# Kernel tuning notes

Hardware: AMD Instinct MI355X
Metric: run time of the kernel (lower is better)

## Reference

```python
import jax, jax.numpy as jnp
import numpy as np

B, T, V, D, H, HS, FF, L = 4, 1024, 32000, 1024, 16, 64, 4096, 8
STD = 0.02

def _ln(x, g, b, eps=1e-5):
    m = x.mean(-1, keepdims=True)
    v = ((x - m) ** 2).mean(-1, keepdims=True)
    return (x - m) / jnp.sqrt(v + eps) * g + b

def setup_inputs() -> dict:
    key = jax.random.key(0)
    ks = jax.random.split(key, 16)
    n = lambda k, shp: jax.random.normal(k, shp, dtype=jnp.float32) * STD
    inp = {
        "idx": jax.random.randint(ks[0], (B, T), 0, V),
        "tok_emb": n(ks[1], (V, D)),
        "pos_emb": n(ks[2], (T, D)),
        # per-layer stacked attention weights; [D, H, HS] per layer (no bias)
        "Wq": n(ks[3], (L, D, H, HS)),
        "Wk": n(ks[4], (L, D, H, HS)),
        "Wv": n(ks[5], (L, D, H, HS)),
        "Wp": n(ks[6], (L, H * HS, D)),
        "bp": jnp.zeros((L, D), jnp.float32),
        "ln1_g": jnp.ones((L, D), jnp.float32),
        "ln1_b": jnp.zeros((L, D), jnp.float32),
        "ln2_g": jnp.ones((L, D), jnp.float32),
        "ln2_b": jnp.zeros((L, D), jnp.float32),
        "W1": n(ks[7], (L, D, FF)),
        "b1": jnp.zeros((L, FF), jnp.float32),
        "W2": n(ks[8], (L, FF, D)),
        "b2": jnp.zeros((L, D), jnp.float32),
        "lnf_g": jnp.ones((D,), jnp.float32),
        "lnf_b": jnp.zeros((D,), jnp.float32),
        "Wlm": n(ks[9], (D, V)),
        "blm": jnp.zeros((V,), jnp.float32),
    }
    return inp

def reference(idx, tok_emb, pos_emb, Wq, Wk, Wv, Wp, bp, ln1_g, ln1_b,
              ln2_g, ln2_b, W1, b1, W2, b2, lnf_g, lnf_b, Wlm, blm):
    Bb, Tt = idx.shape
    x = tok_emb[idx] + pos_emb[:Tt]                      # [B,T,D]
    causal = jnp.tril(jnp.ones((Tt, Tt), bool))          # tril mask
    for l in range(L):
        xn = _ln(x, ln1_g[l], ln1_b[l])
        q = jnp.einsum('btd,dhk->bhtk', xn, Wq[l])
        k = jnp.einsum('btd,dhk->bhtk', xn, Wk[l])
        v = jnp.einsum('btd,dhk->bhtk', xn, Wv[l])
        w = jnp.einsum('bhtk,bhsk->bhts', q, k) * (HS ** -0.5)
        w = jnp.where(causal, w, -jnp.inf)
        w = jax.nn.softmax(w, axis=-1)
        o = jnp.einsum('bhts,bhsk->bhtk', w, v)
        o = o.transpose(0, 2, 1, 3).reshape(Bb, Tt, H * HS)  # concat heads
        x = x + o @ Wp[l] + bp[l]
        xn = _ln(x, ln2_g[l], ln2_b[l])
        x = x + jax.nn.relu(xn @ W1[l] + b1[l]) @ W2[l] + b2[l]
    x = _ln(x, lnf_g, lnf_b)
    logits = x @ Wlm + blm                               # [B,T,V]
    return logits
```

## Files before the change

kernel.cpp:

```cpp
#include <hip/hip_runtime.h>
#include <cstdint>

typedef __attribute__((ext_vector_type(4))) float f32x4;
typedef __attribute__((ext_vector_type(8))) short s16x8;
typedef __attribute__((ext_vector_type(4))) short s16x4;
typedef unsigned short u16;
typedef unsigned int u32;
typedef __attribute__((address_space(1))) void gas_void;
typedef __attribute__((address_space(3))) void las_void;

#define B_ 4
#define T_ 1024
#define V_ 32000
#define D_ 1024
#define H_ 16
#define HS_ 64
#define FF_ 4096
#define L_ 8
#define BT_ (B_ * T_)

__device__ __forceinline__ float bf2f(u16 h) { return __uint_as_float(((u32)h) << 16); }
__device__ __forceinline__ u16 f2bf(float f) {
  u32 u = __float_as_uint(f);
  u += 0x7fffu + ((u >> 16) & 1u);
  return (u16)(u >> 16);
}

__device__ __forceinline__ void gld16(const void* g, void* l) {
  __builtin_amdgcn_global_load_lds((gas_void*)(uintptr_t)g,
                                   (las_void*)(u32)(uintptr_t)l, 16, 0, 0);
}


template <int EPI>
__global__ __launch_bounds__(512, 2) void gemm256(
    const u16* __restrict__ A, const u16* __restrict__ Bt,
    const float* __restrict__ bias, float* Cf, u16* Cb,
    int M, int N, int K, int nrowb) {
  __shared__ u16 lds[2][2][2][8192];
  const int tid = threadIdx.x;
  const int lane = tid & 63;
  const int lr = lane & 15, hi = lane >> 4;
  const int wid = tid >> 6;
  const int wm128 = (wid >> 2) << 7;
  const int wn64 = (wid & 3) << 6;
  const int logical = ((int)blockIdx.x & 7) * ((int)gridDim.x >> 3) + ((int)blockIdx.x >> 3);
  const int row0 = (logical % nrowb) << 8;
  const int col0 = (logical / nrowb) << 8;
  const int NT = K >> 6;
  const int srow = tid >> 2;
  const int schunk = tid & 3;
  const int xo = ((hi + (lr >> 1)) & 3) << 4;

  f32x4 acc[32];
#pragma unroll
  for (int i = 0; i < 32; ++i) acc[i] = f32x4{0.f, 0.f, 0.f, 0.f};
  s16x8 bfr[4];

#define VMW(N) asm volatile("s_waitcnt vmcnt(" #N ")" ::: "memory")

#define STG(DB, DK, OP, KT)                                                    \
  {                                                                            \
    const u16* sp_ = (OP) ? Bt : A;                                            \
    const int base_ = (OP) ? col0 : row0;                                      \
    const int c0_ = ((KT) << 6) + ((DK) << 5);                                 \
    _Pragma("unroll")                                                          \
    for (int sh_ = 0; sh_ < 2; ++sh_) {                                        \
      const int rr_ = (sh_ << 7) + srow;                                       \
      const int ko_ = ((schunk - (rr_ >> 1)) & 3) << 3;                        \
      gld16(sp_ + (size_t)(base_ + rr_) * K + c0_ + ko_,                       \
            (char*)&lds[DB][DK][OP][0] + (sh_ << 13) + (wid << 10));           \
    }                                                                          \
  }

#define PHASE(BUF, MH, KS, LOADB, STG_STMT, VM_STMT)                           \
  {                                                                            \
    __builtin_amdgcn_sched_barrier(0);                                         \
    const char* As_ = (const char*)&lds[BUF][KS][0][0];                        \
    const char* Bs_ = (const char*)&lds[BUF][KS][1][0];                        \
    const int ra_ = wm128 + ((MH) << 6) + lr;                                  \
    s16x8 af_[4];                                                              \
    _Pragma("unroll")                                                          \
    for (int q_ = 0; q_ < 4; ++q_)                                             \
      af_[q_] = *(const s16x8*)(As_ + ((ra_ + (q_ << 4)) << 6) + xo);          \
    if (LOADB) {                                                               \
      _Pragma("unroll")                                                        \
      for (int q_ = 0; q_ < 4; ++q_)                                           \
        bfr[q_] = *(const s16x8*)(Bs_ + ((wn64 + lr + (q_ << 4)) << 6) + xo);  \
    }                                                                          \
    STG_STMT;                                                                  \
    __builtin_amdgcn_sched_barrier(0);                                         \
    __builtin_amdgcn_s_barrier();                                              \
    asm volatile("s_waitcnt lgkmcnt(0)" ::: "memory");                         \
    __builtin_amdgcn_sched_barrier(0);                                         \
    __builtin_amdgcn_s_setprio(1);                                             \
    _Pragma("unroll")                                                          \
    for (int mi_ = 0; mi_ < 4; ++mi_) {                                        \
      _Pragma("unroll")                                                        \
      for (int nj_ = 0; nj_ < 4; ++nj_)                                        \
        acc[((MH)*4 + mi_) * 4 + nj_] = __builtin_amdgcn_mfma_f32_16x16x32_bf16( \
            af_[mi_], bfr[nj_], acc[((MH)*4 + mi_) * 4 + nj_], 0, 0, 0);       \
    }                                                                          \
    __builtin_amdgcn_s_setprio(0);                                             \
    __builtin_amdgcn_sched_barrier(0);                                         \
    VM_STMT;                                                                   \
    __builtin_amdgcn_s_barrier();                                              \
  }

  STG(0, 0, 0, 0)
  STG(0, 0, 1, 0)
  STG(0, 1, 0, 0)
  STG(0, 1, 1, 0)
  STG(1, 0, 0, 1)
  STG(1, 0, 1, 1)
  VMW(8);
  __builtin_amdgcn_s_barrier();

  const int NI = NT >> 1;
  for (int it = 0; it < NI - 1; ++it) {
    const int t1 = 2 * it + 1, t2 = 2 * it + 2, t3 = 2 * it + 3;
    PHASE(0, 0, 0, 1, STG(1, 1, 0, t1), )
    PHASE(0, 1, 0, 0, STG(1, 1, 1, t1), VMW(6))
    PHASE(0, 0, 1, 1, STG(0, 0, 0, t2), )
    PHASE(0, 1, 1, 0, STG(0, 0, 1, t2), VMW(6))
    PHASE(1, 0, 0, 1, STG(0, 1, 0, t2), )
    PHASE(1, 1, 0, 0, STG(0, 1, 1, t2), VMW(6))
    PHASE(1, 0, 1, 1, STG(1, 0, 0, t3), )
    PHASE(1, 1, 1, 0, STG(1, 0, 1, t3), VMW(6))
  }
  {
    PHASE(0, 0, 0, 1, STG(1, 1, 0, NT - 1), )
    PHASE(0, 1, 0, 0, STG(1, 1, 1, NT - 1), VMW(8))
    PHASE(0, 0, 1, 1, (void)0, )
    PHASE(0, 1, 1, 0, (void)0, VMW(4))
    PHASE(1, 0, 0, 1, (void)0, )
    PHASE(1, 1, 0, 0, (void)0, VMW(0))
    PHASE(1, 0, 1, 1, (void)0, )
    PHASE(1, 1, 1, 0, (void)0, )
  }
#undef PHASE
#undef STG
#undef VMW

  const int gr0 = row0 + wm128;
  const int gc0 = col0 + wn64;
#pragma unroll
  for (int nj = 0; nj < 4; ++nj) {
    const int col = gc0 + (nj << 4) + lr;
    const float bv = (EPI != 0) ? bias[col] : 0.f;
#pragma unroll
    for (int mi = 0; mi < 8; ++mi) {
#pragma unroll
      for (int rg = 0; rg < 4; ++rg) {
        const int row = gr0 + (mi << 4) + (hi << 2) + rg;
        const size_t off = (size_t)row * N + col;
        float val = acc[mi * 4 + nj][rg] + bv;
        if constexpr (EPI == 2) val = fmaxf(val, 0.f);
        if constexpr (EPI == 0 || EPI == 2) Cb[off] = f2bf(val);
        else Cf[off] = val;
      }
    }
  }
}

template <int EPI>
__global__ __launch_bounds__(256) void gemm_bt(
    const u16* __restrict__ A, const u16* __restrict__ Bt,
    const float* __restrict__ bias, float* Cf, u16* Cb,
    int M, int N, int K) {
  __shared__ u16 lds[2][2][4096];
  const int tid = threadIdx.x;
  const int lane = tid & 63;
  const int lr = lane & 15, hi = lane >> 4;
  const int wid = tid >> 6;
  const int wm = wid >> 1, wn = wid & 1;
  const int row0 = blockIdx.y << 7, col0 = blockIdx.x << 7;
  const int NT = K >> 5;
  const int wbase = (tid & ~63) << 4;
  const int xo = ((hi + (lr >> 1)) & 3) << 4;

  f32x4 acc[4][4];
#pragma unroll
  for (int i = 0; i < 4; ++i)
#pragma unroll
    for (int j = 0; j < 4; ++j) acc[i][j] = f32x4{0.f, 0.f, 0.f, 0.f};

  auto stage = [&](int buf, int kt) {
#pragma unroll
    for (int c = 0; c < 2; ++c) {
      const int o = (c << 12) + (tid << 4);
      const int r = o >> 6;
      const int ko = ((((o >> 4) & 3) - (r >> 1)) & 3) << 3;
      gld16(A + (size_t)(row0 + r) * K + (kt << 5) + ko,
            (char*)&lds[buf][0][0] + (c << 12) + wbase);
      gld16(Bt + (size_t)(col0 + r) * K + (kt << 5) + ko,
            (char*)&lds[buf][1][0] + (c << 12) + wbase);
    }
  };

  stage(0, 0);
  __syncthreads();
  int cur = 0;
  for (int kt = 0; kt < NT; ++kt) {
    if (kt + 1 < NT) stage(cur ^ 1, kt + 1);
    const char* As = (const char*)&lds[cur][0][0];
    const char* Bs = (const char*)&lds[cur][1][0];
    s16x8 af[4], bfr[4];
#pragma unroll
    for (int i = 0; i < 4; ++i) {
      const int ra = (wm << 6) + (i << 4) + lr;
      af[i] = *(const s16x8*)(As + (ra << 6) + xo);
      const int rb = (wn << 6) + (i << 4) + lr;
      bfr[i] = *(const s16x8*)(Bs + (rb << 6) + xo);
    }
#pragma unroll
    for (int i = 0; i < 4; ++i)
#pragma unroll
      for (int j = 0; j < 4; ++j)
        acc[i][j] =
            __builtin_amdgcn_mfma_f32_16x16x32_bf16(af[i], bfr[j], acc[i][j], 0, 0, 0);
    __syncthreads();
    cur ^= 1;
  }

  const int gr = row0 + (wm << 6);
  const int gc = col0 + (wn << 6);
#pragma unroll
  for (int j = 0; j < 4; ++j) {
    const int col = gc + (j << 4) + lr;
    const float bv = (EPI != 0) ? bias[col] : 0.f;
#pragma unroll
    for (int i = 0; i < 4; ++i) {
#pragma unroll
      for (int rg = 0; rg < 4; ++rg) {
        const int row = gr + (i << 4) + (hi << 2) + rg;
        const size_t off = (size_t)row * N + col;
        float val = acc[i][j][rg] + bv;
        if constexpr (EPI == 1) val += Cf[off];
        if constexpr (EPI == 2) val = fmaxf(val, 0.f);
        if constexpr (EPI == 0 || EPI == 2) Cb[off] = f2bf(val);
        else Cf[off] = val;
      }
    }
  }
}

template <int EPI>
__global__ __launch_bounds__(256) void gemm_bt64(
    const u16* __restrict__ A, const u16* __restrict__ Bt,
    const float* __restrict__ bias, float* Cf, u16* Cb,
    int M, int N, int K) {
  __shared__ u16 lds[2][6144];
  const int tid = threadIdx.x;
  const int lane = tid & 63;
  const int lr = lane & 15, hi = lane >> 4;
  const int w = tid >> 6;
  const int row0 = blockIdx.y << 6, col0 = blockIdx.x << 7;
  const int NT = K >> 5;
  const int wbase = (tid & ~63) << 4;
  const int schunk = tid & 3;
  const int xo = ((hi + (lr >> 1)) & 3) << 4;

  f32x4 acc[4][2];
#pragma unroll
  for (int i = 0; i < 4; ++i)
#pragma unroll
    for (int j = 0; j < 2; ++j) acc[i][j] = f32x4{0.f, 0.f, 0.f, 0.f};

  auto stage = [&](int buf, int kt) {
    const int r = tid >> 2;
    {
      const int ko = ((schunk - (r >> 1)) & 3) << 3;
      gld16(A + (size_t)(row0 + r) * K + (kt << 5) + ko,
            (char*)&lds[buf][0] + wbase);
    }
#pragma unroll
    for (int sh = 0; sh < 2; ++sh) {
      const int rb = (sh << 6) + r;
      const int ko = ((schunk - (rb >> 1)) & 3) << 3;
      gld16(Bt + (size_t)(col0 + rb) * K + (kt << 5) + ko,
            (char*)&lds[buf][2048] + (sh << 12) + wbase);
    }
  };

  stage(0, 0);
  __syncthreads();
  int cur = 0;
  for (int kt = 0; kt < NT; ++kt) {
    if (kt + 1 < NT) stage(cur ^ 1, kt + 1);
    const char* As = (const char*)&lds[cur][0];
    const char* Bs = (const char*)&lds[cur][2048];
    s16x8 af[4], bf2[2];
#pragma unroll
    for (int i = 0; i < 4; ++i)
      af[i] = *(const s16x8*)(As + (((i << 4) + lr) << 6) + xo);
#pragma unroll
    for (int j = 0; j < 2; ++j)
      bf2[j] = *(const s16x8*)(Bs + (((w << 5) + (j << 4) + lr) << 6) + xo);
#pragma unroll
    for (int i = 0; i < 4; ++i)
#pragma unroll
      for (int j = 0; j < 2; ++j)
        acc[i][j] =
            __builtin_amdgcn_mfma_f32_16x16x32_bf16(af[i], bf2[j], acc[i][j], 0, 0, 0);
    __syncthreads();
    cur ^= 1;
  }

  const int gc = col0 + (w << 5);
#pragma unroll
  for (int j = 0; j < 2; ++j) {
    const int col = gc + (j << 4) + lr;
    const float bv = (EPI != 0) ? bias[col] : 0.f;
#pragma unroll
    for (int i = 0; i < 4; ++i) {
#pragma unroll
      for (int rg = 0; rg < 4; ++rg) {
        const int row = row0 + (i << 4) + (hi << 2) + rg;
        const size_t off = (size_t)row * N + col;
        float val = acc[i][j][rg] + bv;
        if constexpr (EPI == 1) val += Cf[off];
        if constexpr (EPI == 2) val = fmaxf(val, 0.f);
        if constexpr (EPI == 0 || EPI == 2) Cb[off] = f2bf(val);
        else Cf[off] = val;
      }
    }
  }
}

__global__ __launch_bounds__(256) void ln_kernel(const float* __restrict__ x,
                                                 const float* __restrict__ gw,
                                                 const float* __restrict__ bw,
                                                 u16* __restrict__ out) {
  const int lane = threadIdx.x & 63;
  const size_t r = ((size_t)blockIdx.x << 2) + (threadIdx.x >> 6);
  const float* xp = x + (r << 10);
  f32x4 v[4];
  float s = 0.f, q = 0.f;
#pragma unroll
  for (int j = 0; j < 4; ++j) {
    v[j] = *(const f32x4*)(xp + (lane << 2) + (j << 8));
#pragma unroll
    for (int e = 0; e < 4; ++e) {
      s += v[j][e];
      q += v[j][e] * v[j][e];
    }
  }
#pragma unroll
  for (int off = 32; off; off >>= 1) {
    s += __shfl_xor(s, off);
    q += __shfl_xor(q, off);
  }
  const float mean = s * (1.f / 1024.f);
  const float var = q * (1.f / 1024.f) - mean * mean;
  const float rstd = rsqrtf(var + 1e-5f);
  u16* op = out + (r << 10);
#pragma unroll
  for (int j = 0; j < 4; ++j) {
    const f32x4 g4 = *(const f32x4*)(gw + (lane << 2) + (j << 8));
    const f32x4 b4 = *(const f32x4*)(bw + (lane << 2) + (j << 8));
    s16x4 o4;
#pragma unroll
    for (int e = 0; e < 4; ++e)
      o4[e] = (short)f2bf((v[j][e] - mean) * rstd * g4[e] + b4[e]);
    *(s16x4*)(op + (lane << 2) + (j << 8)) = o4;
  }
}

__global__ __launch_bounds__(256) void embed_kernel(const int* __restrict__ idx,
                                                    const float* __restrict__ tok,
                                                    const float* __restrict__ pos,
                                                    float* __restrict__ x) {
  const int r = blockIdx.x, tid = threadIdx.x;
  const int t = r & (T_ - 1);
  const int tk = idx[r];
  f32x4 a = *(const f32x4*)(tok + ((size_t)tk << 10) + (tid << 2));
  f32x4 p = *(const f32x4*)(pos + ((size_t)t << 10) + (tid << 2));
  *(f32x4*)(x + ((size_t)r << 10) + (tid << 2)) = a + p;
}

#define TCONV_BODY(SRC, DST, KK, NN)                                           \
  {                                                                            \
    __shared__ float tile[64][65];                                             \
    const int tid = threadIdx.x;                                               \
    const int n0 = blockIdx.x << 6, k0 = blockIdx.y << 6;                      \
    _Pragma("unroll")                                                          \
    for (int it = 0; it < 4; ++it) {                                           \
      const int k = (tid >> 4) + (it << 4);                                    \
      const int n = (tid & 15) << 2;                                           \
      *(f32x4*)&tile[k][n] =                                                   \
          *(const f32x4*)((SRC) + (size_t)(k0 + k) * (NN) + n0 + n);           \
    }                                                                          \
    __syncthreads();                                                           \
    _Pragma("unroll")                                                          \
    for (int it = 0; it < 2; ++it) {                                           \
      const int n = (tid >> 3) + (it << 5);                                    \
      const int kp = (tid & 7) << 3;                                           \
      s16x8 o;                                                                 \
      _Pragma("unroll")                                                        \
      for (int j = 0; j < 8; ++j) o[j] = (short)f2bf(tile[kp + j][n]);         \
      *(s16x8*)((DST) + (size_t)(n0 + n) * (KK) + k0 + kp) = o;                \
    }                                                                          \
  }

__global__ __launch_bounds__(256) void tconv_qkvp(
    const float* __restrict__ Wq, const float* __restrict__ Wk,
    const float* __restrict__ Wv, const float* __restrict__ Wp,
    u16* __restrict__ WqkvT, u16* __restrict__ WpT) {
  const int z = blockIdx.z;
  const int l = z >> 2, m = z & 3;
  const float* src;
  u16* dst;
  if (m == 0) { src = Wq + (size_t)l * D_ * D_; dst = WqkvT + (size_t)l * 3072 * D_; }
  else if (m == 1) { src = Wk + (size_t)l * D_ * D_; dst = WqkvT + (size_t)l * 3072 * D_ + D_ * D_; }
  else if (m == 2) { src = Wv + (size_t)l * D_ * D_; dst = WqkvT + (size_t)l * 3072 * D_ + 2 * D_ * D_; }
  else { src = Wp + (size_t)l * D_ * D_; dst = WpT + (size_t)l * D_ * D_; }
  TCONV_BODY(src, dst, D_, D_)
}

__global__ __launch_bounds__(256) void tconv_w1(const float* __restrict__ W1,
                                                u16* __restrict__ W1T) {
  const int l = blockIdx.z;
  TCONV_BODY(W1 + (size_t)l * D_ * FF_, W1T + (size_t)l * FF_ * D_, D_, FF_)
}

__global__ __launch_bounds__(256) void tconv_w2(const float* __restrict__ W2,
                                                u16* __restrict__ W2T) {
  const int l = blockIdx.z;
  TCONV_BODY(W2 + (size_t)l * FF_ * D_, W2T + (size_t)l * D_ * FF_, FF_, D_)
}

__global__ __launch_bounds__(256) void tconv_kernel(const float* __restrict__ src,
                                                    u16* __restrict__ dst, int K, int N) {
  TCONV_BODY(src, dst, K, N)
}

__global__ __launch_bounds__(512, 4) void fattn_kernel(const u16* __restrict__ qkv,
                                                       u16* __restrict__ o) {
  const int flat = (int)blockIdx.x;
  const int xcd = flat & 7, seq = flat >> 3;
  const int pair = (xcd << 3) + (seq >> 3);
  const int qt = seq & 7;
  const int h = pair & 15, b = pair >> 4;
  const int tid = threadIdx.x;
  const int lane = tid & 63;
  const int lr = lane & 15, hi = lane >> 4;
  const int w = tid >> 6;
  __shared__ alignas(16) u16 Kl[2][4096];
  __shared__ alignas(16) u16 Vt[2][4096];

  const size_t bT = (size_t)(b * T_);
  const int q_row = (qt << 7) + (w << 4) + lr;
  const int qtw = (qt << 1) + (w >> 2);
  const size_t qbase = (bT + q_row) * 3072 + (h << 6);
  s16x8 aq[2];
  aq[0] = *(const s16x8*)(qkv + qbase + hi * 8);
  aq[1] = *(const s16x8*)(qkv + qbase + 32 + hi * 8);

  f32x4 ofr[4];
#pragma unroll
  for (int j = 0; j < 4; ++j) ofr[j] = f32x4{0.f, 0.f, 0.f, 0.f};
  float mrun = -1e30f, lsum = 0.f;
  const float SCL = 0.125f * 1.44269504f;

  uint4 vr0;

#define STAGEK(BUF, KT)                                                        \
  {                                                                            \
    const int r_ = tid >> 3;                                                   \
    const int il_ = (((tid & 7) << 4)) ^ ((r_ & 7) << 4);                      \
    gld16(qkv + (bT + ((KT) << 6) + r_) * 3072 + 1024 + (h << 6) + (il_ >> 1), \
          (char*)&Kl[BUF][0] + ((tid & 448) << 4));                            \
  }
#define LOADV(KT)                                                              \
  {                                                                            \
    vr0 = *(const uint4*)(qkv + (bT + ((KT) << 6) + lane) * 3072 + 2048 +      \
                          (h << 6) + (w << 3));                                \
  }
#define WRITEV(BUF)                                                            \
  {                                                                            \
    const u16* p0_ = (const u16*)&vr0;                                         \
    _Pragma("unroll")                                                          \
    for (int j_ = 0; j_ < 8; ++j_)                                             \
      Vt[BUF][(((w << 3) + j_) << 6) + (lane ^ (j_ << 3))] = p0_[j_];          \
  }

  STAGEK(0, 0)
  LOADV(0)
  asm volatile("s_waitcnt vmcnt(0)" ::: "memory");
  WRITEV(0)
  asm volatile("s_waitcnt lgkmcnt(0)" ::: "memory");
  __builtin_amdgcn_sched_barrier(0);
  __builtin_amdgcn_s_barrier();

  const int nkt = (qt << 1) + 2;
  int cur = 0;
  for (int kt = 0; kt < nkt; ++kt) {
    if (kt + 1 < nkt) {
      STAGEK(cur ^ 1, kt + 1)
      LOADV(kt + 1)
    }

    const bool full = (kt > qtw);
    f32x4 s[4];
    if (!full) {
#pragma unroll
      for (int j = 0; j < 4; ++j) s[j] = f32x4{0.f, 0.f, 0.f, 0.f};
      __builtin_amdgcn_s_setprio(1);
#pragma unroll
      for (int kk = 0; kk < 2; ++kk)
#pragma unroll
        for (int j = 0; j < 4; ++j) {
          const int rb = (j << 4) + lr;
          const s16x8 bk = *(const s16x8*)((const char*)&Kl[cur][0] + (rb << 7) +
                                           ((((kk << 2) + hi) ^ (rb & 7)) << 4));
          s[j] = __builtin_amdgcn_mfma_f32_16x16x32_bf16(bk, aq[kk], s[j], 0, 0, 0);
        }
      __builtin_amdgcn_s_setprio(0);
      if (kt == qtw) {
        const int qr = q_row & 63;
#pragma unroll
        for (int j = 0; j < 4; ++j)
#pragma unroll
          for (int rg = 0; rg < 4; ++rg) {
            const int kvr = (j << 4) + (hi << 2) + rg;
            s[j][rg] = (kvr > qr) ? -1e30f : s[j][rg] * SCL;
          }
      } else {
#pragma unroll
        for (int j = 0; j < 4; ++j) s[j] = s[j] * SCL;
      }
    } else {
#pragma unroll
      for (int j = 0; j < 4; ++j) s[j] = f32x4{-1e30f, -1e30f, -1e30f, -1e30f};
    }

    float mx = fmaxf(fmaxf(s[0][0], s[0][1]), fmaxf(s[0][2], s[0][3]));
#pragma unroll
    for (int j = 1; j < 4; ++j)
#pragma unroll
      for (int rg = 0; rg < 4; ++rg) mx = fmaxf(mx, s[j][rg]);
    mx = fmaxf(mx, __shfl_xor(mx, 16));
    mx = fmaxf(mx, __shfl_xor(mx, 32));
    const float mn = fmaxf(mrun, mx);
    const float sc = exp2f(mrun - mn);
    mrun = mn;
    float rs = 0.f;
#pragma unroll
    for (int j = 0; j < 4; ++j)
#pragma unroll
      for (int rg = 0; rg < 4; ++rg) {
        const float e = exp2f(s[j][rg] - mn);
        s[j][rg] = e;
        rs += e;
      }
    rs += __shfl_xor(rs, 16);
    rs += __shfl_xor(rs, 32);
    lsum = lsum * sc + rs;
    float scO[4];
#pragma unroll
    for (int rg = 0; rg < 4; ++rg) scO[rg] = __shfl(sc, (hi << 2) + rg);
#pragma unroll
    for (int j2 = 0; j2 < 4; ++j2)
#pragma unroll
      for (int rg = 0; rg < 4; ++rg) ofr[j2][rg] *= scO[rg];

    if (!full) {
      s16x8 pb[2];
#pragma unroll
      for (int kk = 0; kk < 2; ++kk)
#pragma unroll
        for (int i = 0; i < 4; ++i) {
          pb[kk][i] = (short)f2bf(s[2 * kk][i]);
          pb[kk][4 + i] = (short)f2bf(s[2 * kk + 1][i]);
        }

      __builtin_amdgcn_s_setprio(1);
#pragma unroll
      for (int kk = 0; kk < 2; ++kk)
#pragma unroll
        for (int j2 = 0; j2 < 4; ++j2) {
          const int drow = (j2 << 4) + lr;
          const int swz = (drow & 7) << 3;
          const int base = drow << 6;
          const s16x4 lo = *(const s16x4*)&Vt[cur][base + (((kk << 5) + (hi << 2)) ^ swz)];
          const s16x4 hv = *(const s16x4*)&Vt[cur][base + (((kk << 5) + 16 + (hi << 2)) ^ swz)];
          const s16x8 vb = __builtin_shufflevector(lo, hv, 0, 1, 2, 3, 4, 5, 6, 7);
          ofr[j2] = __builtin_amdgcn_mfma_f32_16x16x32_bf16(pb[kk], vb, ofr[j2], 0, 0, 0);
        }
      __builtin_amdgcn_s_setprio(0);
    }

    if (kt + 1 < nkt) {
      asm volatile("s_waitcnt vmcnt(0)" ::: "memory");
      WRITEV(cur ^ 1)
    }
    asm volatile("s_waitcnt lgkmcnt(0)" ::: "memory");
    __builtin_amdgcn_sched_barrier(0);
    __builtin_amdgcn_s_barrier();
    cur ^= 1;
  }

  const float rinv = 1.f / lsum;
  float rO[4];
#pragma unroll
  for (int rg = 0; rg < 4; ++rg) rO[rg] = __shfl(rinv, (hi << 2) + rg);
#pragma unroll
  for (int j2 = 0; j2 < 4; ++j2)
#pragma unroll
    for (int rg = 0; rg < 4; ++rg) {
      const int row = (qt << 7) + (w << 4) + (hi << 2) + rg;
      const int col = (h << 6) + (j2 << 4) + lr;
      o[(bT + row) * 1024 + col] = f2bf(ofr[j2][rg] * rO[rg]);
    }
#undef STAGEK
#undef LOADV
#undef WRITEV
}

extern "C" void kernel_launch(void* const* d_in, const int* in_sizes, int n_in,
                              void* d_out, int out_size, void* d_ws, size_t ws_size,
                              hipStream_t stream) {
  (void)in_sizes; (void)n_in; (void)out_size; (void)ws_size;
  const int* idx = (const int*)d_in[0];
  const float* tokE = (const float*)d_in[1];
  const float* posE = (const float*)d_in[2];
  const float* Wq = (const float*)d_in[3];
  const float* Wk = (const float*)d_in[4];
  const float* Wv = (const float*)d_in[5];
  const float* Wp = (const float*)d_in[6];
  const float* bp = (const float*)d_in[7];
  const float* ln1g = (const float*)d_in[8];
  const float* ln1b = (const float*)d_in[9];
  const float* ln2g = (const float*)d_in[10];
  const float* ln2b = (const float*)d_in[11];
  const float* W1 = (const float*)d_in[12];
  const float* b1 = (const float*)d_in[13];
  const float* W2 = (const float*)d_in[14];
  const float* b2 = (const float*)d_in[15];
  const float* lnfg = (const float*)d_in[16];
  const float* lnfb = (const float*)d_in[17];
  const float* Wlm = (const float*)d_in[18];
  const float* blm = (const float*)d_in[19];

  char* p = (char*)d_ws;
  float* x = (float*)p;   p += (size_t)BT_ * D_ * 4;
  u16* xn = (u16*)p;      p += (size_t)BT_ * D_ * 2;
  u16* qkv = (u16*)p;     p += (size_t)BT_ * 3072 * 2;
  u16* ob = (u16*)p;      p += (size_t)BT_ * D_ * 2;
  u16* hb = (u16*)p;      p += (size_t)BT_ * FF_ * 2;
  u16* WqkvT = (u16*)p;   p += (size_t)L_ * 3072 * D_ * 2;
  u16* WpT = (u16*)p;     p += (size_t)L_ * D_ * D_ * 2;
  u16* W1T = (u16*)p;     p += (size_t)L_ * FF_ * D_ * 2;
  u16* W2T = (u16*)p;     p += (size_t)L_ * D_ * FF_ * 2;
  u16* WlmT = (u16*)p;    p += (size_t)V_ * D_ * 2;

  dim3 blk(256);
  dim3 blk512(512);
  tconv_qkvp<<<dim3(16, 16, 32), blk, 0, stream>>>(Wq, Wk, Wv, Wp, WqkvT, WpT);
  tconv_w1<<<dim3(64, 16, 8), blk, 0, stream>>>(W1, W1T);
  tconv_w2<<<dim3(16, 64, 8), blk, 0, stream>>>(W2, W2T);
  tconv_kernel<<<dim3(500, 16), blk, 0, stream>>>(Wlm, WlmT, D_, V_);

  embed_kernel<<<dim3(BT_), blk, 0, stream>>>(idx, tokE, posE, x);

  for (int l = 0; l < L_; ++l) {
    ln_kernel<<<dim3(BT_ / 4), blk, 0, stream>>>(x, ln1g + l * D_, ln1b + l * D_, xn);
    gemm_bt<0><<<dim3(24, 32), blk, 0, stream>>>(xn, WqkvT + (size_t)l * 3072 * D_,
                                                 nullptr, nullptr, qkv, BT_, 3072, D_);
    fattn_kernel<<<dim3(512), blk512, 0, stream>>>(qkv, ob);
    gemm_bt64<1><<<dim3(8, 64), blk, 0, stream>>>(ob, WpT + (size_t)l * D_ * D_,
                                                  bp + l * D_, x, nullptr, BT_, D_, D_);
    ln_kernel<<<dim3(BT_ / 4), blk, 0, stream>>>(x, ln2g + l * D_, ln2b + l * D_, xn);
    gemm_bt<2><<<dim3(32, 32), blk, 0, stream>>>(xn, W1T + (size_t)l * FF_ * D_,
                                                 b1 + l * FF_, nullptr, hb, BT_, FF_, D_);
    gemm_bt64<1><<<dim3(8, 64), blk, 0, stream>>>(hb, W2T + (size_t)l * D_ * FF_,
                                                  b2 + l * D_, x, nullptr, BT_, D_, FF_);
  }
  ln_kernel<<<dim3(BT_ / 4), blk, 0, stream>>>(x, lnfg, lnfb, xn);
  gemm256<3><<<dim3(2000), blk512, 0, stream>>>(xn, WlmT, blm, (float*)d_out, nullptr,
                                                BT_, V_, D_, 16);
}
```

Before: 2.481 ms.

## Replace residual-add GEMMs with split-K 128x128 tile kernel using atomic accumulation

The Wp and W2 projection GEMMs (N=1024) move from a 64x128 tile kernel that read and rewrote the residual to a 128x128 tile kernel with split-K over grid z (2 splits for Wp, 4 for W2). Each split atomically adds its partial sums straight into the fp32 residual x, and only the first split adds the bias. The goal is more data reuse per tile while keeping enough blocks to fill the GPU, and dropping the separate residual read. In exchange it pays for fp32 atomics and makes the summation order nondeterministic.

```diff
diff --git a/kernel.cpp b/kernel.cpp
--- a/kernel.cpp
+++ b/kernel.cpp
@@ -236,7 +236,6 @@
         const int row = gr + (i << 4) + (hi << 2) + rg;
         const size_t off = (size_t)row * N + col;
         float val = acc[i][j][rg] + bv;
-        if constexpr (EPI == 1) val += Cf[off];
         if constexpr (EPI == 2) val = fmaxf(val, 0.f);
         if constexpr (EPI == 0 || EPI == 2) Cb[off] = f2bf(val);
         else Cf[off] = val;
@@ -245,41 +244,40 @@
   }
 }
 
-template <int EPI>
-__global__ __launch_bounds__(256) void gemm_bt64(
+__global__ __launch_bounds__(256) void gemm_bt_ks(
     const u16* __restrict__ A, const u16* __restrict__ Bt,
-    const float* __restrict__ bias, float* Cf, u16* Cb,
+    const float* __restrict__ bias, float* Cf,
     int M, int N, int K) {
-  __shared__ u16 lds[2][6144];
+  __shared__ u16 lds[2][2][4096];
   const int tid = threadIdx.x;
   const int lane = tid & 63;
   const int lr = lane & 15, hi = lane >> 4;
-  const int w = tid >> 6;
-  const int row0 = blockIdx.y << 6, col0 = blockIdx.x << 7;
-  const int NT = K >> 5;
+  const int wid = tid >> 6;
+  const int wm = wid >> 1, wn = wid & 1;
+  const int row0 = blockIdx.y << 7, col0 = blockIdx.x << 7;
+  const int z = blockIdx.z;
+  const int kc = K / (int)gridDim.z;
+  const int kof = z * kc;
+  const int NT = kc >> 5;
   const int wbase = (tid & ~63) << 4;
-  const int schunk = tid & 3;
   const int xo = ((hi + (lr >> 1)) & 3) << 4;
 
-  f32x4 acc[4][2];
+  f32x4 acc[4][4];
 #pragma unroll
   for (int i = 0; i < 4; ++i)
 #pragma unroll
-    for (int j = 0; j < 2; ++j) acc[i][j] = f32x4{0.f, 0.f, 0.f, 0.f};
+    for (int j = 0; j < 4; ++j) acc[i][j] = f32x4{0.f, 0.f, 0.f, 0.f};
 
   auto stage = [&](int buf, int kt) {
-    const int r = tid >> 2;
-    {
-      const int ko = ((schunk - (r >> 1)) & 3) << 3;
-      gld16(A + (size_t)(row0 + r) * K + (kt << 5) + ko,
-            (char*)&lds[buf][0] + wbase);
-    }
-#pragma unroll
-    for (int sh = 0; sh < 2; ++sh) {
-      const int rb = (sh << 6) + r;
-      const int ko = ((schunk - (rb >> 1)) & 3) << 3;
-      gld16(Bt + (size_t)(col0 + rb) * K + (kt << 5) + ko,
-            (char*)&lds[buf][2048] + (sh << 12) + wbase);
+#pragma unroll
+    for (int c = 0; c < 2; ++c) {
+      const int o = (c << 12) + (tid << 4);
+      const int r = o >> 6;
+      const int ko = ((((o >> 4) & 3) - (r >> 1)) & 3) << 3;
+      gld16(A + (size_t)(row0 + r) * K + kof + (kt << 5) + ko,
+            (char*)&lds[buf][0][0] + (c << 12) + wbase);
+      gld16(Bt + (size_t)(col0 + r) * K + kof + (kt << 5) + ko,
+            (char*)&lds[buf][1][0] + (c << 12) + wbase);
     }
   };
 
@@ -288,41 +286,39 @@
   int cur = 0;
   for (int kt = 0; kt < NT; ++kt) {
     if (kt + 1 < NT) stage(cur ^ 1, kt + 1);
-    const char* As = (const char*)&lds[cur][0];
-    const char* Bs = (const char*)&lds[cur][2048];
-    s16x8 af[4], bf2[2];
+    const char* As = (const char*)&lds[cur][0][0];
+    const char* Bs = (const char*)&lds[cur][1][0];
+    s16x8 af[4], bfr[4];
+#pragma unroll
+    for (int i = 0; i < 4; ++i) {
+      const int ra = (wm << 6) + (i << 4) + lr;
+      af[i] = *(const s16x8*)(As + (ra << 6) + xo);
+      const int rb = (wn << 6) + (i << 4) + lr;
+      bfr[i] = *(const s16x8*)(Bs + (rb << 6) + xo);
+    }
 #pragma unroll
     for (int i = 0; i < 4; ++i)
-      af[i] = *(const s16x8*)(As + (((i << 4) + lr) << 6) + xo);
-#pragma unroll
-    for (int j = 0; j < 2; ++j)
-      bf2[j] = *(const s16x8*)(Bs + (((w << 5) + (j << 4) + lr) << 6) + xo);
-#pragma unroll
-    for (int i = 0; i < 4; ++i)
-#pragma unroll
-      for (int j = 0; j < 2; ++j)
+#pragma unroll
+      for (int j = 0; j < 4; ++j)
         acc[i][j] =
-            __builtin_amdgcn_mfma_f32_16x16x32_bf16(af[i], bf2[j], acc[i][j], 0, 0, 0);
+            __builtin_amdgcn_mfma_f32_16x16x32_bf16(af[i], bfr[j], acc[i][j], 0, 0, 0);
     __syncthreads();
     cur ^= 1;
   }
 
-  const int gc = col0 + (w << 5);
-#pragma unroll
-  for (int j = 0; j < 2; ++j) {
+  const int gr = row0 + (wm << 6);
+  const int gc = col0 + (wn << 6);
+  const bool addb = (z == 0);
+#pragma unroll
+  for (int j = 0; j < 4; ++j) {
     const int col = gc + (j << 4) + lr;
-    const float bv = (EPI != 0) ? bias[col] : 0.f;
+    const float bv = addb ? bias[col] : 0.f;
 #pragma unroll
     for (int i = 0; i < 4; ++i) {
 #pragma unroll
       for (int rg = 0; rg < 4; ++rg) {
-        const int row = row0 + (i << 4) + (hi << 2) + rg;
-        const size_t off = (size_t)row * N + col;
-        float val = acc[i][j][rg] + bv;
-        if constexpr (EPI == 1) val += Cf[off];
-        if constexpr (EPI == 2) val = fmaxf(val, 0.f);
-        if constexpr (EPI == 0 || EPI == 2) Cb[off] = f2bf(val);
-        else Cf[off] = val;
+        const int row = gr + (i << 4) + (hi << 2) + rg;
+        atomicAdd(&Cf[(size_t)row * N + col], acc[i][j][rg] + bv);
       }
     }
   }
@@ -669,13 +665,13 @@
     gemm_bt<0><<<dim3(24, 32), blk, 0, stream>>>(xn, WqkvT + (size_t)l * 3072 * D_,
                                                  nullptr, nullptr, qkv, BT_, 3072, D_);
     fattn_kernel<<<dim3(512), blk512, 0, stream>>>(qkv, ob);
-    gemm_bt64<1><<<dim3(8, 64), blk, 0, stream>>>(ob, WpT + (size_t)l * D_ * D_,
-                                                  bp + l * D_, x, nullptr, BT_, D_, D_);
+    gemm_bt_ks<<<dim3(8, 32, 2), blk, 0, stream>>>(ob, WpT + (size_t)l * D_ * D_,
+                                                   bp + l * D_, x, BT_, D_, D_);
     ln_kernel<<<dim3(BT_ / 4), blk, 0, stream>>>(x, ln2g + l * D_, ln2b + l * D_, xn);
     gemm_bt<2><<<dim3(32, 32), blk, 0, stream>>>(xn, W1T + (size_t)l * FF_ * D_,
                                                  b1 + l * FF_, nullptr, hb, BT_, FF_, D_);
-    gemm_bt64<1><<<dim3(8, 64), blk, 0, stream>>>(hb, W2T + (size_t)l * D_ * FF_,
-                                                  b2 + l * D_, x, nullptr, BT_, D_, FF_);
+    gemm_bt_ks<<<dim3(8, 32, 4), blk, 0, stream>>>(hb, W2T + (size_t)l * D_ * FF_,
+                                                   b2 + l * D_, x, BT_, D_, FF_);
   }
   ln_kernel<<<dim3(BT_ / 4), blk, 0, stream>>>(x, lnfg, lnfb, xn);
   gemm256<3><<<dim3(2000), blk512, 0, stream>>>(xn, WlmT, blm, (float*)d_out, nullptr,
```

Result: slower. 2.741 ms (+10.5%).
